# Kernel tuning notes

Hardware: AMD Instinct MI355X
Metric: run time of the kernel (lower is better)

The kernel has to match this reference:

```python
import jax, jax.numpy as jnp
import numpy as np
from jax import lax

V = 500000  # vocab
B = 4096    # batch_num (fixed at init via h0/c0)
E = 64      # embed_size_word
H = 64      # lstm hidden


def setup_inputs() -> dict:
    key = jax.random.key(0)
    ks = iter(jax.random.split(key, 40))
    nrm = lambda *s: 0.1 * jax.random.normal(next(ks), s, dtype=jnp.float32)
    x = jax.random.randint(next(ks), (912, B), 0, V).astype(jnp.float32)
    return dict(
        x=x,
        word_embed=nrm(V, E),
        lstm_Wih=nrm(4, 4 * H, E), lstm_Whh=nrm(4, 4 * H, H),
        lstm_bih=nrm(4, 4 * H), lstm_bhh=nrm(4, 4 * H),
        h0=nrm(4, B, H), c0=nrm(4, B, H),
        w_l=nrm(4, H, H), b_l=jnp.zeros((4, H, 1), jnp.float32),
        conv1_w=nrm(12, 1, 2, E), conv1_b=jnp.zeros((12,), jnp.float32),
        lin1_w=nrm(64, 24), lin1_b=jnp.zeros((64,), jnp.float32),
        conv2_w=nrm(12, 1, 2, E), conv2_b=jnp.zeros((12,), jnp.float32),
        lin2_w=nrm(64, 24), lin2_b=jnp.zeros((64,), jnp.float32),
        wide_w=nrm(64, 81), wide_b=jnp.zeros((64, 1), jnp.float32),
        cq_w=nrm(64, 64 * 7), cq_b=jnp.zeros((64, 1), jnp.float32),
        cqu_w=nrm(64, 128), cqu_b=jnp.zeros((64, 1), jnp.float32),
        dw_w=nrm(1, 64), dw_b=jnp.zeros((1, 1), jnp.float32),
    )


def _masked_mean(terms_f, table):
    # terms_f: [rows, B] float ids. Faithful to torch: L = sum(sign(all terms)),
    # L = L if L > 1 else 1, then mean over first min(L, rows) rows.
    rows = terms_f.shape[0]
    emb = table[terms_f.astype(jnp.int32)]                    # [rows, B, E]
    n = jnp.sum(jnp.sign(terms_f))
    L = jnp.minimum(jnp.where(n > 1, n, 1.0), float(rows))
    mask = (jnp.arange(rows, dtype=jnp.float32) < L)[:, None, None]
    return jnp.sum(emb * mask, axis=0) / L                    # [B, E]


def _lstm_last(x_seq, h0, c0, Wih, Whh, bih, bhh):
    # PyTorch LSTM (i,f,g,o gate order); returns last-step output h_T. x_seq: [T,B,E]
    def step(carry, xt):
        h, c = carry
        g = xt @ Wih.T + h @ Whh.T + bih + bhh                # [B, 4H]
        i, f, gg, o = jnp.split(g, 4, axis=-1)
        c = jax.nn.sigmoid(f) * c + jax.nn.sigmoid(i) * jnp.tanh(gg)
        h = jax.nn.sigmoid(o) * jnp.tanh(c)
        return (h, c), None
    (h, _), _ = lax.scan(step, (h0, c0), x_seq)
    return h                                                  # [B, H]


def reference(x, word_embed, lstm_Wih, lstm_Whh, lstm_bih, lstm_bhh, h0, c0, w_l, b_l,
              conv1_w, conv1_b, lin1_w, lin1_b, conv2_w, conv2_b, lin2_w, lin2_b,
              wide_w, wide_b, cq_w, cq_b, cqu_w, cqu_b, dw_w, dw_b):
    Bn = x.shape[1]
    wide_feat = x[:81]
    user_item_seq = x[81:276]
    query_feat = x[276:292]
    user_query_seq = x[292:462]
    query_item_query = x[462:562]
    user_query_item = x[562:662]
    user_item_query = x[662:812]
    query_user_item = x[812:]

    q_sum = _masked_mean(query_feat[:10], word_embed).T       # [64, B]

    def step_means(seg, chunk, term_rows):
        # split seg into 5 chunks of `chunk` rows, embed first `term_rows` rows per chunk
        chunks = seg.reshape(5, chunk, Bn)[:, :term_rows]     # [5, term_rows, B]
        return jax.vmap(lambda t: _masked_mean(t, word_embed))(chunks)  # [5, B, E]

    def lstm_stream(steps, i):
        h = _lstm_last(steps, h0[i], c0[i], lstm_Wih[i], lstm_Whh[i], lstm_bih[i], lstm_bhh[i])
        return jnp.tanh(w_l[i] @ h.T + b_l[i])                # [64, B]

    s1 = lstm_stream(step_means(user_item_seq[-65:], 13, 10), 0)
    s2 = lstm_stream(step_means(user_item_query[:50], 10, 5), 1)
    s3 = lstm_stream(step_means(user_query_item[-50:], 10, 5), 2)
    s4 = lstm_stream(step_means(user_query_seq[-65:], 13, 10), 3)

    def cnn_stream(steps, cw, cb, lw, lb):
        xi = steps.transpose(1, 0, 2)[:, None]                # [B, 1, 5, E]
        y = lax.conv_general_dilated(xi, cw, (1, 1), 'VALID',
                dimension_numbers=('NCHW', 'OIHW', 'NCHW')) + cb[None, :, None, None]
        y = jax.nn.relu(y)                                    # [B, 12, 4, 1]
        y = lax.reduce_window(y, -jnp.inf, lax.max, (1, 1, 2, 1), (1, 1, 2, 1), 'VALID')
        y = y.transpose(0, 2, 3, 1).reshape(Bn, 24)           # [B, 2*1*12]
        return jax.nn.relu(y @ lw.T + lb).T                   # [64, B]

    c1 = cnn_stream(step_means(query_item_query[-50:], 10, 5), conv1_w, conv1_b, lin1_w, lin1_b)
    c2 = cnn_stream(step_means(query_user_item[-50:], 10, 5), conv2_w, conv2_b, lin2_w, lin2_b)

    wide = jnp.tanh(wide_w @ wide_feat + wide_b)              # [64, B]
    q = jnp.tanh(cq_w @ jnp.concatenate([q_sum, s1, s2, s3, s4, c1, c2], 0) + cq_b)
    qw = jnp.tanh(cqu_w @ jnp.concatenate([q, wide], 0) + cqu_b)
    return dw_w @ qw + dw_b                                   # [1, B] logits
```

## Files before the change

kernel.cpp:

```cpp
#include <hip/hip_runtime.h>
#include <math.h>

#define BN 4096
typedef unsigned short u16;
typedef unsigned int   u32;
typedef short bfx8 __attribute__((ext_vector_type(8)));
typedef float fx4  __attribute__((ext_vector_type(4)));

__device__ const int c_base[31] = {
  276,
  211, 224, 237, 250, 263,
  662, 672, 682, 692, 702,
  612, 622, 632, 642, 652,
  397, 410, 423, 436, 449,
  512, 522, 532, 542, 552,
  862, 872, 882, 892, 902
};
__device__ const int c_rows[31] = {
  10,
  10,10,10,10,10,
  5,5,5,5,5,
  5,5,5,5,5,
  10,10,10,10,10,
  5,5,5,5,5,
  5,5,5,5,5
};

__device__ __forceinline__ u16 f2bf(float f){
  u32 u = __float_as_uint(f);
  return (u16)((u + 0x7FFFu + ((u >> 16) & 1u)) >> 16);
}
__device__ __forceinline__ float bf2f(u16 h){ return __uint_as_float(((u32)h) << 16); }
__device__ __forceinline__ float4 ld4(const float* p){ return *(const float4*)p; }
__device__ __forceinline__ float dot4(float4 a, float4 b){
  return a.x*b.x + a.y*b.y + a.z*b.z + a.w*b.w;
}
__device__ __forceinline__ float sigf(float v){ return 1.0f / (1.0f + __expf(-v)); }

extern "C" __global__ __launch_bounds__(256)
void count_kernel(const float* __restrict__ x, int* __restrict__ cnt){
  __shared__ int red[256];
  const int c = blockIdx.x >> 3, part = blockIdx.x & 7;
  const int base = c_base[c], rows = c_rows[c];
  const int n_per = rows * 512;
  const int start = part * n_per;
  int s = 0;
  for (int i = start + threadIdx.x; i < start + n_per; i += 256){
    float v = x[(size_t)(base + (i >> 12)) * BN + (i & 4095)];
    s += (v > 0.f) ? 1 : ((v < 0.f) ? -1 : 0);
  }
  red[threadIdx.x] = s; __syncthreads();
  for (int off = 128; off > 0; off >>= 1){
    if (threadIdx.x < off) red[threadIdx.x] += red[threadIdx.x + off];
    __syncthreads();
  }
  if (threadIdx.x == 0) atomicAdd(&cnt[c], red[0]);
}

extern "C" __global__ __launch_bounds__(256)
void prep_kernel(const float* __restrict__ Wih, const float* __restrict__ Whh,
                 const float* __restrict__ wl,  const float* __restrict__ bih,
                 const float* __restrict__ bhh,
                 u16* __restrict__ Wcb, u16* __restrict__ wlb, float* __restrict__ bias_sum){
  int idx = blockIdx.x * 256 + threadIdx.x;
  if (idx < 131072){
    int s = idx >> 15, rem = idx & 32767, n = rem >> 7, k = rem & 127;
    float v = (k < 64) ? Wih[s*16384 + n*64 + k] : Whh[s*16384 + n*64 + (k-64)];
    Wcb[idx] = f2bf(v);
  } else if (idx < 147456){
    int j = idx - 131072;
    wlb[j] = f2bf(wl[j]);
  } else if (idx < 148480){
    int j = idx - 147456;
    bias_sum[j] = bih[j] + bhh[j];
  }
}

__device__ __forceinline__ void gather4(const float* __restrict__ x,
                                        const float* __restrict__ we,
                                        float L, int base, int rows,
                                        int b0, int lane, float* m) {
  float a0 = 0.f, a1 = 0.f, a2 = 0.f, a3 = 0.f;
  for (int r = 0; r < rows; ++r) {
    if ((float)r < L) {
      float4 iv = ld4(x + (size_t)(base + r) * BN + b0);
      a0 += we[(size_t)(int)iv.x * 64 + lane];
      a1 += we[(size_t)(int)iv.y * 64 + lane];
      a2 += we[(size_t)(int)iv.z * 64 + lane];
      a3 += we[(size_t)(int)iv.w * 64 + lane];
    }
  }
  m[0] = a0 / L; m[1] = a1 / L; m[2] = a2 / L; m[3] = a3 / L;
}

extern "C" __global__ __launch_bounds__(256)
void means_kernel(const float* __restrict__ x, const float* __restrict__ we,
                  const int* __restrict__ cnt, u16* __restrict__ Mbf){
  const int c = blockIdx.x >> 8, tile = blockIdx.x & 255;
  const int w = threadIdx.x >> 6, lane = threadIdx.x & 63;
  const int b0 = tile * 16 + w * 4;
  const int base = c_base[c], rows = c_rows[c];
  const float L = fminf(fmaxf((float)cnt[c], 1.f), (float)rows);
  float m[4];
  gather4(x, we, L, base, rows, b0, lane, m);
  #pragma unroll
  for (int j = 0; j < 4; ++j)
    Mbf[((size_t)c * BN + b0 + j) * 64 + lane] = f2bf(m[j]);
}

extern "C" __global__ __launch_bounds__(256, 1)
void lstm_kernel(const u16* __restrict__ Wcb, const u16* __restrict__ wlb,
                 const float* __restrict__ bias_sum, const u16* __restrict__ Mbf,
                 const float* __restrict__ h0, const float* __restrict__ c0,
                 const float* __restrict__ bl, float* __restrict__ S){
  __shared__ u16 Xh[64][136];

  const int tid = threadIdx.x, w = tid >> 6, lane = tid & 63;
  const int quad = lane >> 4, l0 = lane & 15;
  const int st = blockIdx.x & 3, tile = blockIdx.x >> 2, b0 = tile * 64;
  const int brow = 16 * w + l0;
  const u16* Wc = Wcb + (size_t)st * 32768;

  fx4 bias4[16];
  #pragma unroll
  for (int mt = 0; mt < 16; ++mt)
    bias4[mt] = *(const fx4*)(bias_sum + st*256 + mt*16 + quad*4);

  float cst[4][4];
  #pragma unroll
  for (int dc = 0; dc < 4; ++dc){
    float4 v = ld4(c0 + ((size_t)st*BN + b0 + brow)*64 + dc*16 + quad*4);
    cst[dc][0]=v.x; cst[dc][1]=v.y; cst[dc][2]=v.z; cst[dc][3]=v.w;
  }
  {
    const float* hp = h0 + ((size_t)st*BN + b0 + brow)*64 + quad*16;
    #pragma unroll
    for (int i = 0; i < 4; ++i){
      float4 v = ld4(hp + i*4);
      u32* dst = (u32*)&Xh[brow][64 + quad*16 + i*4];
      dst[0] = (u32)f2bf(v.x) | ((u32)f2bf(v.y) << 16);
      dst[1] = (u32)f2bf(v.z) | ((u32)f2bf(v.w) << 16);
    }
  }

  for (int t = 0; t < 5; ++t){
    {
      const u16* src = Mbf + ((size_t)(1 + st*5 + t)*BN + b0 + brow)*64 + quad*16;
      *(uint4*)&Xh[brow][quad*16]     = *(const uint4*)src;
      *(uint4*)&Xh[brow][quad*16 + 8] = *(const uint4*)(src + 8);
    }
    __syncthreads();

    fx4 acc[16];
    #pragma unroll
    for (int mt = 0; mt < 16; ++mt) acc[mt] = bias4[mt];
    #pragma unroll
    for (int kc = 0; kc < 4; ++kc){
      bfx8 bfr = *(const bfx8*)&Xh[brow][kc*32 + quad*8];
      #pragma unroll
      for (int mt = 0; mt < 16; ++mt){
        bfx8 afr = *(const bfx8*)(Wc + (size_t)(mt*16 + l0)*128 + kc*32 + quad*8);
        acc[mt] = __builtin_amdgcn_mfma_f32_16x16x32_bf16(afr, bfr, acc[mt], 0, 0, 0);
      }
    }
    #pragma unroll
    for (int dc = 0; dc < 4; ++dc){
      u16 hv[4];
      #pragma unroll
      for (int r = 0; r < 4; ++r){
        float ig = sigf(acc[dc][r]);
        float fg = sigf(acc[4 + dc][r]);
        float gg = tanhf(acc[8 + dc][r]);
        float og = sigf(acc[12 + dc][r]);
        float cc = fg * cst[dc][r] + ig * gg;
        cst[dc][r] = cc;
        hv[r] = f2bf(og * tanhf(cc));
      }
      u32* dst = (u32*)&Xh[brow][64 + dc*16 + quad*4];
      dst[0] = (u32)hv[0] | ((u32)hv[1] << 16);
      dst[1] = (u32)hv[2] | ((u32)hv[3] << 16);
    }
    __syncthreads();
  }

  fx4 acc2[4];
  #pragma unroll
  for (int mt = 0; mt < 4; ++mt){ acc2[mt].x=0.f; acc2[mt].y=0.f; acc2[mt].z=0.f; acc2[mt].w=0.f; }
  #pragma unroll
  for (int kc = 0; kc < 2; ++kc){
    bfx8 bfr = *(const bfx8*)&Xh[brow][64 + kc*32 + quad*8];
    #pragma unroll
    for (int mt = 0; mt < 4; ++mt){
      bfx8 afr = *(const bfx8*)(wlb + (size_t)st*4096 + (size_t)(mt*16 + l0)*64 + kc*32 + quad*8);
      acc2[mt] = __builtin_amdgcn_mfma_f32_16x16x32_bf16(afr, bfr, acc2[mt], 0, 0, 0);
    }
  }
  #pragma unroll
  for (int mt = 0; mt < 4; ++mt){
    fx4 blv = *(const fx4*)(bl + st*64 + mt*16 + quad*4);
    fx4 o;
    o.x = tanhf(acc2[mt].x + blv.x);
    o.y = tanhf(acc2[mt].y + blv.y);
    o.z = tanhf(acc2[mt].z + blv.z);
    o.w = tanhf(acc2[mt].w + blv.w);
    *(fx4*)(S + ((size_t)st*BN + b0 + brow)*64 + mt*16 + quad*4) = o;
  }
}

extern "C" __global__ __launch_bounds__(256)
void final_kernel(
    const float* __restrict__ x,   const u16* __restrict__ Mbf,
    const float* __restrict__ S,
    const float* __restrict__ c1w, const float* __restrict__ c1b,
    const float* __restrict__ l1w, const float* __restrict__ l1b,
    const float* __restrict__ c2w, const float* __restrict__ c2b,
    const float* __restrict__ l2w, const float* __restrict__ l2b,
    const float* __restrict__ ww,  const float* __restrict__ wb,
    const float* __restrict__ cqw, const float* __restrict__ cqb,
    const float* __restrict__ cquw,const float* __restrict__ cqub,
    const float* __restrict__ dww, const float* __restrict__ dwb,
    float* __restrict__ out)
{
  __shared__ __align__(16) float cbuf[4][448];
  __shared__ __align__(16) float sbuf[4][320];
  __shared__ __align__(16) float abuf[4][128];

  const int tid = threadIdx.x, w = tid >> 6, lane = tid & 63;
  const int b = blockIdx.x * 4 + w;

  cbuf[w][lane] = bf2f(Mbf[(size_t)b * 64 + lane]);
  #pragma unroll
  for (int s = 0; s < 4; ++s)
    cbuf[w][64 + s*64 + lane] = S[((size_t)s*BN + b)*64 + lane];

  for (int cs = 0; cs < 2; ++cs){
    const float* cw = cs ? c2w : c1w;
    const float* cb = cs ? c2b : c1b;
    const float* lw = cs ? l2w : l1w;
    const float* lb = cs ? l2b : l1b;
    const int chunk0 = 21 + cs * 5;

    #pragma unroll
    for (int t = 0; t < 5; ++t)
      sbuf[w][t*64 + lane] = bf2f(Mbf[((size_t)(chunk0 + t)*BN + b)*64 + lane]);
    __syncthreads();

    const int o  = lane >> 2;
    const int hh = lane & 3;
    float a = 0.f;
    if (lane < 48){
      a = cb[o];
      #pragma unroll
      for (int kh = 0; kh < 2; ++kh)
        #pragma unroll 4
        for (int kq = 0; kq < 16; ++kq){
          const int k4 = kq * 4;
          float4 sv = *(const float4*)&sbuf[w][(hh + kh)*64 + k4];
          float4 cv = ld4(cw + (size_t)o*128 + kh*64 + k4);
          a += dot4(sv, cv);
        }
      a = fmaxf(a, 0.f);
    }
    __syncthreads();
    abuf[w][lane] = a;
    __syncthreads();

    float a2 = lb[lane];
    #pragma unroll
    for (int p = 0; p < 2; ++p)
      #pragma unroll
      for (int o2 = 0; o2 < 12; ++o2){
        float f = fmaxf(abuf[w][o2*4 + 2*p], abuf[w][o2*4 + 2*p + 1]);
        a2 += lw[lane*24 + p*12 + o2] * f;
      }
    cbuf[w][(5 + cs)*64 + lane] = fmaxf(a2, 0.f);
    __syncthreads();
  }

  float accw = wb[lane];
  for (int i = 0; i < 81; ++i)
    accw += ww[lane*81 + i] * x[(size_t)i * BN + b];
  float widev = tanhf(accw);

  __syncthreads();
  float accq = cqb[lane];
  #pragma unroll 4
  for (int kq = 0; kq < 112; ++kq){
    const int k4 = kq * 4;
    accq += dot4(ld4(cqw + (size_t)lane*448 + k4), *(const float4*)&cbuf[w][k4]);
  }
  float qv = tanhf(accq);

  __syncthreads();
  abuf[w][lane]      = qv;
  abuf[w][64 + lane] = widev;
  __syncthreads();

  float accu = cqub[lane];
  #pragma unroll 4
  for (int kq = 0; kq < 32; ++kq){
    const int k4 = kq * 4;
    accu += dot4(ld4(cquw + (size_t)lane*128 + k4), *(const float4*)&abuf[w][k4]);
  }

  float pj = dww[lane] * tanhf(accu);
  #pragma unroll
  for (int off = 32; off > 0; off >>= 1) pj += __shfl_down(pj, off);
  if (lane == 0) out[b] = pj + dwb[0];
}

extern "C" void kernel_launch(void* const* d_in, const int* in_sizes, int n_in,
                              void* d_out, int out_size, void* d_ws, size_t ws_size,
                              hipStream_t stream) {
  const float* x    = (const float*)d_in[0];
  const float* we   = (const float*)d_in[1];
  const float* Wih  = (const float*)d_in[2];
  const float* Whh  = (const float*)d_in[3];
  const float* bihp = (const float*)d_in[4];
  const float* bhhp = (const float*)d_in[5];
  const float* h0   = (const float*)d_in[6];
  const float* c0   = (const float*)d_in[7];
  const float* wl   = (const float*)d_in[8];
  const float* bl   = (const float*)d_in[9];
  const float* c1w  = (const float*)d_in[10];
  const float* c1b  = (const float*)d_in[11];
  const float* l1w  = (const float*)d_in[12];
  const float* l1b  = (const float*)d_in[13];
  const float* c2w  = (const float*)d_in[14];
  const float* c2b  = (const float*)d_in[15];
  const float* l2w  = (const float*)d_in[16];
  const float* l2b  = (const float*)d_in[17];
  const float* ww   = (const float*)d_in[18];
  const float* wb   = (const float*)d_in[19];
  const float* cqw  = (const float*)d_in[20];
  const float* cqb  = (const float*)d_in[21];
  const float* cquw = (const float*)d_in[22];
  const float* cqub = (const float*)d_in[23];
  const float* dww  = (const float*)d_in[24];
  const float* dwb  = (const float*)d_in[25];

  char* ws = (char*)d_ws;
  int*   cnt  = (int*)ws;
  u16*   Mbf  = (u16*)(ws + 1024);
  u16*   Wcb  = (u16*)(ws + 16253952);
  u16*   wlb  = (u16*)(ws + 16516096);
  float* bias = (float*)(ws + 16548864);
  float* S    = (float*)(ws + 16552960);

  hipMemsetAsync(cnt, 0, 31 * sizeof(int), stream);
  count_kernel<<<248, 256, 0, stream>>>(x, cnt);
  prep_kernel<<<580, 256, 0, stream>>>(Wih, Whh, wl, bihp, bhhp, Wcb, wlb, bias);
  means_kernel<<<7936, 256, 0, stream>>>(x, we, cnt, Mbf);
  lstm_kernel<<<256, 256, 0, stream>>>(Wcb, wlb, bias, Mbf, h0, c0, bl, S);
  final_kernel<<<1024, 256, 0, stream>>>(x, Mbf, S,
      c1w, c1b, l1w, l1b, c2w, c2b, l2w, l2b,
      ww, wb, cqw, cqb, cquw, cqub, dww, dwb, (float*)d_out);
}
```

Baseline: 386.2 us.

## Restructure final kernel for batch-tiled weight reuse, merge setup kernels, unroll means

Merges the count and weight-prep kernels into one setup launch, which also pre-transposes the dense-head weights so loads are contiguous along outputs. The final kernel is rewritten so each block handles 8 batch columns and each thread computes two outputs across them, reusing weight loads across batches via shared-memory activation tiles. The means gather is templated on row count and fully unrolled with multiplicative masking, which increases loads in flight but always reads every row even when masked. Adds extra setup work and shared-memory pressure in the final kernel.

```diff
diff --git a/kernel.cpp b/kernel.cpp
--- a/kernel.cpp
+++ b/kernel.cpp
@@ -32,37 +32,40 @@
 }
 __device__ __forceinline__ float bf2f(u16 h){ return __uint_as_float(((u32)h) << 16); }
 __device__ __forceinline__ float4 ld4(const float* p){ return *(const float4*)p; }
-__device__ __forceinline__ float dot4(float4 a, float4 b){
-  return a.x*b.x + a.y*b.y + a.z*b.z + a.w*b.w;
-}
 __device__ __forceinline__ float sigf(float v){ return 1.0f / (1.0f + __expf(-v)); }
 
 extern "C" __global__ __launch_bounds__(256)
-void count_kernel(const float* __restrict__ x, int* __restrict__ cnt){
+void setup_kernel(const float* __restrict__ x, int* __restrict__ cnt,
+                  const float* __restrict__ Wih, const float* __restrict__ Whh,
+                  const float* __restrict__ wl,  const float* __restrict__ bih,
+                  const float* __restrict__ bhh,
+                  const float* __restrict__ cqw, const float* __restrict__ cquw,
+                  const float* __restrict__ ww,  const float* __restrict__ l1w,
+                  const float* __restrict__ l2w,
+                  u16* __restrict__ Wcb, u16* __restrict__ wlb,
+                  float* __restrict__ bias_sum,
+                  float* __restrict__ cqwT, float* __restrict__ cquwT,
+                  float* __restrict__ wwT,  float* __restrict__ lwT){
   __shared__ int red[256];
-  const int c = blockIdx.x >> 3, part = blockIdx.x & 7;
-  const int base = c_base[c], rows = c_rows[c];
-  const int n_per = rows * 512;
-  const int start = part * n_per;
-  int s = 0;
-  for (int i = start + threadIdx.x; i < start + n_per; i += 256){
-    float v = x[(size_t)(base + (i >> 12)) * BN + (i & 4095)];
-    s += (v > 0.f) ? 1 : ((v < 0.f) ? -1 : 0);
-  }
-  red[threadIdx.x] = s; __syncthreads();
-  for (int off = 128; off > 0; off >>= 1){
-    if (threadIdx.x < off) red[threadIdx.x] += red[threadIdx.x + off];
-    __syncthreads();
-  }
-  if (threadIdx.x == 0) atomicAdd(&cnt[c], red[0]);
-}
-
-extern "C" __global__ __launch_bounds__(256)
-void prep_kernel(const float* __restrict__ Wih, const float* __restrict__ Whh,
-                 const float* __restrict__ wl,  const float* __restrict__ bih,
-                 const float* __restrict__ bhh,
-                 u16* __restrict__ Wcb, u16* __restrict__ wlb, float* __restrict__ bias_sum){
-  int idx = blockIdx.x * 256 + threadIdx.x;
+  if (blockIdx.x < 248){
+    const int c = blockIdx.x >> 3, part = blockIdx.x & 7;
+    const int base = c_base[c], rows = c_rows[c];
+    const int n_per = rows * 512;
+    const int start = part * n_per;
+    int s = 0;
+    for (int i = start + threadIdx.x; i < start + n_per; i += 256){
+      float v = x[(size_t)(base + (i >> 12)) * BN + (i & 4095)];
+      s += (v > 0.f) ? 1 : ((v < 0.f) ? -1 : 0);
+    }
+    red[threadIdx.x] = s; __syncthreads();
+    for (int off = 128; off > 0; off >>= 1){
+      if (threadIdx.x < off) red[threadIdx.x] += red[threadIdx.x + off];
+      __syncthreads();
+    }
+    if (threadIdx.x == 0) atomicAdd(&cnt[c], red[0]);
+    return;
+  }
+  int idx = (blockIdx.x - 248) * 256 + threadIdx.x;
   if (idx < 131072){
     int s = idx >> 15, rem = idx & 32767, n = rem >> 7, k = rem & 127;
     float v = (k < 64) ? Wih[s*16384 + n*64 + k] : Whh[s*16384 + n*64 + (k-64)];
@@ -73,22 +76,41 @@
   } else if (idx < 148480){
     int j = idx - 147456;
     bias_sum[j] = bih[j] + bhh[j];
-  }
-}
-
-__device__ __forceinline__ void gather4(const float* __restrict__ x,
-                                        const float* __restrict__ we,
-                                        float L, int base, int rows,
-                                        int b0, int lane, float* m) {
+  } else if (idx < 177152){
+    int j = idx - 148480;
+    int k = j >> 6, m = j & 63;
+    cqwT[j] = cqw[m*448 + k];
+  } else if (idx < 185344){
+    int j = idx - 177152;
+    int k = j >> 6, m = j & 63;
+    cquwT[j] = cquw[m*128 + k];
+  } else if (idx < 190528){
+    int j = idx - 185344;
+    int k = j >> 6, m = j & 63;
+    wwT[j] = ww[m*81 + k];
+  } else if (idx < 193600){
+    int j = idx - 190528;
+    int cs = j >= 1536;
+    int r = j - (cs ? 1536 : 0);
+    int k = r >> 6, m = r & 63;
+    lwT[j] = (cs ? l2w : l1w)[m*24 + k];
+  }
+}
+
+template<int ROWS>
+__device__ __forceinline__ void means_body(const float* __restrict__ x,
+                                           const float* __restrict__ we,
+                                           float L, int base, int b0, int lane,
+                                           float* m){
   float a0 = 0.f, a1 = 0.f, a2 = 0.f, a3 = 0.f;
-  for (int r = 0; r < rows; ++r) {
-    if ((float)r < L) {
-      float4 iv = ld4(x + (size_t)(base + r) * BN + b0);
-      a0 += we[(size_t)(int)iv.x * 64 + lane];
-      a1 += we[(size_t)(int)iv.y * 64 + lane];
-      a2 += we[(size_t)(int)iv.z * 64 + lane];
-      a3 += we[(size_t)(int)iv.w * 64 + lane];
-    }
+  #pragma unroll
+  for (int r = 0; r < ROWS; ++r){
+    float4 iv = ld4(x + (size_t)(base + r) * BN + b0);
+    float wr = ((float)r < L) ? 1.f : 0.f;
+    a0 += wr * we[(size_t)(int)iv.x * 64 + lane];
+    a1 += wr * we[(size_t)(int)iv.y * 64 + lane];
+    a2 += wr * we[(size_t)(int)iv.z * 64 + lane];
+    a3 += wr * we[(size_t)(int)iv.w * 64 + lane];
   }
   m[0] = a0 / L; m[1] = a1 / L; m[2] = a2 / L; m[3] = a3 / L;
 }
@@ -102,7 +124,8 @@
   const int base = c_base[c], rows = c_rows[c];
   const float L = fminf(fmaxf((float)cnt[c], 1.f), (float)rows);
   float m[4];
-  gather4(x, we, L, base, rows, b0, lane, m);
+  if (rows == 5) means_body<5>(x, we, L, base, b0, lane, m);
+  else          means_body<10>(x, we, L, base, b0, lane, m);
   #pragma unroll
   for (int j = 0; j < 4; ++j)
     Mbf[((size_t)c * BN + b0 + j) * 64 + lane] = f2bf(m[j]);
@@ -212,101 +235,132 @@
     const float* __restrict__ x,   const u16* __restrict__ Mbf,
     const float* __restrict__ S,
     const float* __restrict__ c1w, const float* __restrict__ c1b,
-    const float* __restrict__ l1w, const float* __restrict__ l1b,
     const float* __restrict__ c2w, const float* __restrict__ c2b,
-    const float* __restrict__ l2w, const float* __restrict__ l2b,
-    const float* __restrict__ ww,  const float* __restrict__ wb,
-    const float* __restrict__ cqw, const float* __restrict__ cqb,
-    const float* __restrict__ cquw,const float* __restrict__ cqub,
-    const float* __restrict__ dww, const float* __restrict__ dwb,
-    float* __restrict__ out)
+    const float* __restrict__ l1b, const float* __restrict__ l2b,
+    const float* __restrict__ wwT, const float* __restrict__ wb,
+    const float* __restrict__ cqwT,const float* __restrict__ cqb,
+    const float* __restrict__ cquwT,const float* __restrict__ cqub,
+    const float* __restrict__ lwT, const float* __restrict__ dww,
+    const float* __restrict__ dwb, float* __restrict__ out)
 {
-  __shared__ __align__(16) float cbuf[4][448];
-  __shared__ __align__(16) float sbuf[4][320];
-  __shared__ __align__(16) float abuf[4][128];
-
-  const int tid = threadIdx.x, w = tid >> 6, lane = tid & 63;
-  const int b = blockIdx.x * 4 + w;
-
-  cbuf[w][lane] = bf2f(Mbf[(size_t)b * 64 + lane]);
-  #pragma unroll
-  for (int s = 0; s < 4; ++s)
-    cbuf[w][64 + s*64 + lane] = S[((size_t)s*BN + b)*64 + lane];
+  __shared__ float cb[448][9];
+  __shared__ float qwin[128][9];
+  __shared__ float sm[5][64][9];
+  __shared__ float co[48][9];
+  __shared__ float cwS[12][130];
+  __shared__ float red[32][8];
+
+  const int tid = threadIdx.x;
+  const int b   = tid & 7;
+  const int mg  = tid >> 3;
+  const int b0  = blockIdx.x * 8;
+
+  {
+    const int e = tid & 63, rr = tid >> 6;
+    #pragma unroll
+    for (int i = 0; i < 2; ++i){
+      const int bb = rr*2 + i;
+      cb[e][bb] = bf2f(Mbf[(size_t)(b0 + bb)*64 + e]);
+      #pragma unroll
+      for (int s = 0; s < 4; ++s)
+        cb[64 + s*64 + e][bb] = S[((size_t)s*BN + b0 + bb)*64 + e];
+    }
+  }
+
+  {
+    float a0 = wb[mg*2], a1 = wb[mg*2+1];
+    #pragma unroll 4
+    for (int k = 0; k < 81; ++k){
+      float xv = x[(size_t)k*BN + b0 + b];
+      float2 wv = *(const float2*)(wwT + k*64 + mg*2);
+      a0 += wv.x * xv; a1 += wv.y * xv;
+    }
+    qwin[64 + mg*2][b]     = tanhf(a0);
+    qwin[64 + mg*2 + 1][b] = tanhf(a1);
+  }
 
   for (int cs = 0; cs < 2; ++cs){
-    const float* cw = cs ? c2w : c1w;
-    const float* cb = cs ? c2b : c1b;
-    const float* lw = cs ? l2w : l1w;
-    const float* lb = cs ? l2b : l1b;
-    const int chunk0 = 21 + cs * 5;
-
-    #pragma unroll
-    for (int t = 0; t < 5; ++t)
-      sbuf[w][t*64 + lane] = bf2f(Mbf[((size_t)(chunk0 + t)*BN + b)*64 + lane]);
+    const float* cw    = cs ? c2w : c1w;
+    const float* cbias = cs ? c2b : c1b;
+    const float* lb    = cs ? l2b : l1b;
+
     __syncthreads();
-
-    const int o  = lane >> 2;
-    const int hh = lane & 3;
-    float a = 0.f;
-    if (lane < 48){
-      a = cb[o];
+    {
+      const int e = tid & 63, rr = tid >> 6;
       #pragma unroll
-      for (int kh = 0; kh < 2; ++kh)
-        #pragma unroll 4
-        for (int kq = 0; kq < 16; ++kq){
-          const int k4 = kq * 4;
-          float4 sv = *(const float4*)&sbuf[w][(hh + kh)*64 + k4];
-          float4 cv = ld4(cw + (size_t)o*128 + kh*64 + k4);
-          a += dot4(sv, cv);
+      for (int t = 0; t < 5; ++t)
+        #pragma unroll
+        for (int i = 0; i < 2; ++i){
+          const int bb = rr*2 + i;
+          sm[t][e][bb] = bf2f(Mbf[((size_t)(21 + cs*5 + t)*BN + b0 + bb)*64 + e]);
         }
-      a = fmaxf(a, 0.f);
+      for (int r2 = tid; r2 < 1536; r2 += 256){
+        const int o = r2 >> 7, j = r2 & 127;
+        cwS[o][j] = cw[o*128 + j];
+      }
     }
     __syncthreads();
-    abuf[w][lane] = a;
+
+    if (mg < 24){
+      const int o = mg >> 1, hb = (mg & 1) * 2;
+      float a0 = cbias[o], a1 = cbias[o];
+      #pragma unroll 4
+      for (int e = 0; e < 64; ++e){
+        float w0 = cwS[o][e], w1 = cwS[o][64 + e];
+        float s0 = sm[hb][e][b], s1 = sm[hb+1][e][b], s2 = sm[hb+2][e][b];
+        a0 += w0*s0 + w1*s1;
+        a1 += w0*s1 + w1*s2;
+      }
+      co[o*4 + hb][b]     = fmaxf(a0, 0.f);
+      co[o*4 + hb + 1][b] = fmaxf(a1, 0.f);
+    }
     __syncthreads();
 
-    float a2 = lb[lane];
-    #pragma unroll
-    for (int p = 0; p < 2; ++p)
+    {
+      float a0 = lb[mg*2], a1 = lb[mg*2+1];
       #pragma unroll
-      for (int o2 = 0; o2 < 12; ++o2){
-        float f = fmaxf(abuf[w][o2*4 + 2*p], abuf[w][o2*4 + 2*p + 1]);
-        a2 += lw[lane*24 + p*12 + o2] * f;
+      for (int k = 0; k < 24; ++k){
+        const int p = k >= 12, o = k - (p ? 12 : 0);
+        float f = fmaxf(co[o*4 + 2*p][b], co[o*4 + 2*p + 1][b]);
+        float2 lv = *(const float2*)(lwT + (cs*24 + k)*64 + mg*2);
+        a0 += lv.x * f; a1 += lv.y * f;
       }
-    cbuf[w][(5 + cs)*64 + lane] = fmaxf(a2, 0.f);
-    __syncthreads();
-  }
-
-  float accw = wb[lane];
-  for (int i = 0; i < 81; ++i)
-    accw += ww[lane*81 + i] * x[(size_t)i * BN + b];
-  float widev = tanhf(accw);
+      cb[320 + cs*64 + mg*2][b]     = fmaxf(a0, 0.f);
+      cb[320 + cs*64 + mg*2 + 1][b] = fmaxf(a1, 0.f);
+    }
+  }
 
   __syncthreads();
-  float accq = cqb[lane];
-  #pragma unroll 4
-  for (int kq = 0; kq < 112; ++kq){
-    const int k4 = kq * 4;
-    accq += dot4(ld4(cqw + (size_t)lane*448 + k4), *(const float4*)&cbuf[w][k4]);
-  }
-  float qv = tanhf(accq);
-
+  {
+    float a0 = cqb[mg*2], a1 = cqb[mg*2+1];
+    #pragma unroll 8
+    for (int k = 0; k < 448; ++k){
+      float a = cb[k][b];
+      float2 wv = *(const float2*)(cqwT + k*64 + mg*2);
+      a0 += wv.x * a; a1 += wv.y * a;
+    }
+    qwin[mg*2][b]     = tanhf(a0);
+    qwin[mg*2 + 1][b] = tanhf(a1);
+  }
   __syncthreads();
-  abuf[w][lane]      = qv;
-  abuf[w][64 + lane] = widev;
+  {
+    float a0 = cqub[mg*2], a1 = cqub[mg*2+1];
+    #pragma unroll 8
+    for (int k = 0; k < 128; ++k){
+      float a = qwin[k][b];
+      float2 wv = *(const float2*)(cquwT + k*64 + mg*2);
+      a0 += wv.x * a; a1 += wv.y * a;
+    }
+    float2 dv = *(const float2*)(dww + mg*2);
+    red[mg][b] = dv.x * tanhf(a0) + dv.y * tanhf(a1);
+  }
   __syncthreads();
-
-  float accu = cqub[lane];
-  #pragma unroll 4
-  for (int kq = 0; kq < 32; ++kq){
-    const int k4 = kq * 4;
-    accu += dot4(ld4(cquw + (size_t)lane*128 + k4), *(const float4*)&abuf[w][k4]);
-  }
-
-  float pj = dww[lane] * tanhf(accu);
-  #pragma unroll
-  for (int off = 32; off > 0; off >>= 1) pj += __shfl_down(pj, off);
-  if (lane == 0) out[b] = pj + dwb[0];
+  if (tid < 8){
+    float s = dwb[0];
+    #pragma unroll 8
+    for (int g = 0; g < 32; ++g) s += red[g][tid];
+    out[b0 + tid] = s;
+  }
 }
 
 extern "C" void kernel_launch(void* const* d_in, const int* in_sizes, int n_in,
@@ -340,19 +394,23 @@
   const float* dwb  = (const float*)d_in[25];
 
   char* ws = (char*)d_ws;
-  int*   cnt  = (int*)ws;
-  u16*   Mbf  = (u16*)(ws + 1024);
-  u16*   Wcb  = (u16*)(ws + 16253952);
-  u16*   wlb  = (u16*)(ws + 16516096);
-  float* bias = (float*)(ws + 16548864);
-  float* S    = (float*)(ws + 16552960);
+  int*   cnt   = (int*)ws;
+  u16*   Mbf   = (u16*)(ws + 1024);
+  u16*   Wcb   = (u16*)(ws + 16253952);
+  u16*   wlb   = (u16*)(ws + 16516096);
+  float* bias  = (float*)(ws + 16548864);
+  float* S     = (float*)(ws + 16552960);
+  float* cqwT  = (float*)(ws + 20747264);
+  float* cquwT = (float*)(ws + 20861952);
+  float* wwT   = (float*)(ws + 20894720);
+  float* lwT   = (float*)(ws + 20915456);
 
   hipMemsetAsync(cnt, 0, 31 * sizeof(int), stream);
-  count_kernel<<<248, 256, 0, stream>>>(x, cnt);
-  prep_kernel<<<580, 256, 0, stream>>>(Wih, Whh, wl, bihp, bhhp, Wcb, wlb, bias);
+  setup_kernel<<<1005, 256, 0, stream>>>(x, cnt, Wih, Whh, wl, bihp, bhhp,
+      cqw, cquw, ww, l1w, l2w, Wcb, wlb, bias, cqwT, cquwT, wwT, lwT);
   means_kernel<<<7936, 256, 0, stream>>>(x, we, cnt, Mbf);
   lstm_kernel<<<256, 256, 0, stream>>>(Wcb, wlb, bias, Mbf, h0, c0, bl, S);
-  final_kernel<<<1024, 256, 0, stream>>>(x, Mbf, S,
-      c1w, c1b, l1w, l1b, c2w, c2b, l2w, l2b,
-      ww, wb, cqw, cqb, cquw, cqub, dww, dwb, (float*)d_out);
-}
+  final_kernel<<<512, 256, 0, stream>>>(x, Mbf, S,
+      c1w, c1b, c2w, c2b, l1b, l2b,
+      wwT, wb, cqwT, cqb, cquwT, cqub, lwT, dww, dwb, (float*)d_out);
+}
```

Measured after the change: 354.6 us. -8.2%, faster.
